# Kernel optimization log

Hardware: AMD Instinct MI355X
Metric: run time of the kernel (lower is better)

Reference implementation:

```python
import jax, jax.numpy as jnp
import numpy as np

B, S, F, U = 64, 512, 128, 512          # seq_length == units (required for broadcast in original code)
SIGDIM = F + F * F                       # level-2 truncated signature dimension
GRID_SIZE, SPLINE_ORDER = 5, 3           # efficient-KAN style defaults
NB = GRID_SIZE + SPLINE_ORDER            # number of b-spline basis functions per input feature
LN_EPS = 1e-3                            # keras LayerNormalization default epsilon


def _make_grid():
    h = 2.0 / GRID_SIZE  # uniform grid on [-1, 1], extended by spline order
    return -1.0 + h * jnp.arange(-SPLINE_ORDER, GRID_SIZE + SPLINE_ORDER + 1, dtype=jnp.float32)


def _b_splines(x, grid):
    # x: (N, F) -> (N, F, NB) via Cox-de Boor recursion
    x = x[..., None]
    bases = ((x >= grid[:-1]) & (x < grid[1:])).astype(x.dtype)
    for p in range(1, SPLINE_ORDER + 1):
        left = (x - grid[:-(p + 1)]) / (grid[p:-1] - grid[:-(p + 1)])
        right = (grid[p + 1:] - x) / (grid[p + 1:] - grid[1:-p])
        bases = left * bases[..., :-1] + right * bases[..., 1:]
    return bases


def _kan_linear(x, base_w, spline_w, grid):
    # KANLinear, no bias / no layernorm: silu base branch + b-spline branch
    lead = x.shape[:-1]
    base = jax.nn.silu(x) @ base_w                                  # (..., U)
    b = _b_splines(x.reshape(-1, x.shape[-1]), grid)                # (N, F, NB)
    spl = jnp.einsum('nfk,ufk->nu', b, spline_w).reshape(*lead, base_w.shape[1])
    return base + spl


def _signature2(x):
    # level-2 path signature of piecewise-linear path x: (B, S, F) -> (B, F + F*F)
    dx = x[:, 1:] - x[:, :-1]                                       # (B, S-1, F)
    s1 = dx.sum(axis=1)                                             # (B, F)
    cs = jnp.cumsum(dx, axis=1)
    prev = jnp.concatenate([jnp.zeros_like(cs[:, :1]), cs[:, :-1]], axis=1)
    s2 = jnp.einsum('bti,btj->bij', prev + 0.5 * dx, dx)            # (B, F, F)
    return jnp.concatenate([s1, s2.reshape(x.shape[0], -1)], axis=-1)


def _grkan(sig, w1, b1, w2, b2, w3, b3, w4, b4, ws, bs, gamma, beta):
    # gated residual network mapping signature -> softmax attention weights (B, U)
    h = jax.nn.elu(sig @ w1 + b1)
    h = h @ w2 + b2
    glu = jax.nn.sigmoid(h @ w3 + b3) * (h @ w4 + b4)
    y = sig @ ws + bs + glu
    mu = jnp.mean(y, axis=-1, keepdims=True)
    var = jnp.var(y, axis=-1, keepdims=True)
    y = (y - mu) / jnp.sqrt(var + LN_EPS) * gamma + beta
    return jax.nn.softmax(y, axis=-1)


def setup_inputs() -> dict:
    key = jax.random.key(0)
    ks = jax.random.split(key, 24)
    n = lambda k, shp, s=0.02: jax.random.normal(k, shp, dtype=jnp.float32) * s
    inp = {
        'inputs': jax.random.normal(ks[0], (B, S, F), dtype=jnp.float32),
        'h_prev': jax.random.normal(ks[1], (B, U), dtype=jnp.float32),
        'c_prev': jax.random.normal(ks[2], (B, U), dtype=jnp.float32),
        'time_kernel': n(ks[3], (S, 1), 0.1),
        'kan_base_w': n(ks[4], (F, U)),
        'kan_spline_w': n(ks[5], (U, F, NB)),
        'g_w1': n(ks[6], (SIGDIM, U)), 'g_b1': jnp.zeros((U,), jnp.float32),
        'g_w2': n(ks[7], (U, U)), 'g_b2': jnp.zeros((U,), jnp.float32),
        'g_w3': n(ks[8], (U, U)), 'g_b3': jnp.zeros((U,), jnp.float32),
        'g_w4': n(ks[9], (U, U)), 'g_b4': jnp.zeros((U,), jnp.float32),
        'g_skip_w': n(ks[10], (SIGDIM, U)), 'g_skip_b': jnp.zeros((U,), jnp.float32),
        'ln_gamma': jnp.ones((U,), jnp.float32), 'ln_beta': jnp.zeros((U,), jnp.float32),
        'wf': n(ks[11], (2 * U, U)), 'bf': jnp.zeros((U,), jnp.float32),
        'wi': n(ks[12], (2 * U, U)), 'bi': jnp.zeros((U,), jnp.float32),
        'wc': n(ks[13], (2 * U, U)), 'bc': jnp.zeros((U,), jnp.float32),
        'wo': n(ks[14], (2 * U, U)), 'bo': jnp.zeros((U,), jnp.float32),
    }
    return inp


def reference(inputs, h_prev, c_prev, time_kernel, kan_base_w, kan_spline_w,
              g_w1, g_b1, g_w2, g_b2, g_w3, g_b3, g_w4, g_b4, g_skip_w, g_skip_b,
              ln_gamma, ln_beta, wf, bf, wi, bi, wc, bc, wo, bo):
    grid = _make_grid()
    weighted = time_kernel * inputs                                  # (B,S,F)
    sig = _signature2(weighted)                                      # (B,SIGDIM)
    attn = _grkan(sig, g_w1, g_b1, g_w2, g_b2, g_w3, g_b3, g_w4, g_b4,
                  g_skip_w, g_skip_b, ln_gamma, ln_beta)             # (B,S) since U==S
    kan_out = _kan_linear(weighted, kan_base_w, kan_spline_w, grid)  # (B,S,U)
    attended = kan_out * attn[..., None]                             # (B,S,U)
    current = attended.mean(axis=1)                                  # (B,U)
    combined = jnp.concatenate([current, h_prev], axis=-1)           # (B,2U)
    f = jax.nn.sigmoid(combined @ wf + bf)
    i = jax.nn.sigmoid(combined @ wi + bi)
    cand = jnp.tanh(combined @ wc + bc)
    o = jax.nn.sigmoid(combined @ wo + bo)
    c_new = f * c_prev + i * cand
    h_new = o * jnp.tanh(c_new)
    return h_new, c_new
```

## Files before the change

kernel.cpp:

```cpp
#include <hip/hip_runtime.h>
#include <math.h>

#define BB 64
#define SS 512
#define FF 128
#define UU 512
#define SIGDIM (FF + FF*FF)
#define K3 16512
#define KK 1152
#define SIG_KC 43
#define SIG_STEPS 6

typedef __attribute__((ext_vector_type(8))) __bf16 bf16x8;
typedef __attribute__((ext_vector_type(8))) unsigned short u16x8;
typedef __attribute__((ext_vector_type(4))) float f32x4;

__device__ __forceinline__ unsigned short f2bf(float x) {
    unsigned int u = __float_as_uint(x);
    unsigned int r = u + 0x7FFFu + ((u >> 16) & 1u);
    return (unsigned short)(r >> 16);
}

__device__ __forceinline__ float sigmoidf(float x) { return 1.0f / (1.0f + expf(-x)); }

__global__ __launch_bounds__(256) void k_prep(const float* __restrict__ splw,
                                              const float* __restrict__ basew,
                                              const float* __restrict__ h_prev,
                                              const float* __restrict__ w2, const float* __restrict__ w3,
                                              const float* __restrict__ w4, const float* __restrict__ wf,
                                              const float* __restrict__ wi, const float* __restrict__ wc,
                                              const float* __restrict__ wo,
                                              unsigned short* __restrict__ Wt,
                                              unsigned short* __restrict__ comb_b,
                                              unsigned short* __restrict__ W2t,
                                              unsigned short* __restrict__ W3t,
                                              unsigned short* __restrict__ W4t,
                                              unsigned short* __restrict__ Wgt) {
    int z = blockIdx.z;
    int tid = threadIdx.x;
    if (z == 0) {
        int base = (blockIdx.y * 16 + blockIdx.x) * 256 + tid;
        {
            int b = base >> 9, uu = base & 511;
            comb_b[(size_t)b * 1024 + 512 + uu] = f2bf(h_prev[base]);
        }
        for (int idx = base; idx < UU * KK; idx += 128 * 256) {
            int u = idx / KK, c = idx % KK;
            float v = (c < 1024) ? splw[(size_t)u * 1024 + c] : basew[(size_t)(c - 1024) * UU + u];
            Wt[idx] = f2bf(v);
        }
        return;
    }
    int zz = z - 1;
    int Kdim = (zz < 3) ? 512 : 1024;
    int kt = blockIdx.x, ut = blockIdx.y;
    if (kt * 64 >= Kdim) return;
    const float* src;
    unsigned short* dst;
    switch (zz) {
        case 0: src = w2; dst = W2t; break;
        case 1: src = w3; dst = W3t; break;
        case 2: src = w4; dst = W4t; break;
        case 3: src = wf; dst = Wgt; break;
        case 4: src = wi; dst = Wgt + (size_t)512 * 1024; break;
        case 5: src = wc; dst = Wgt + (size_t)1024 * 1024; break;
        default: src = wo; dst = Wgt + (size_t)1536 * 1024; break;
    }
    __shared__ float tile[64][67];
    int k0 = kt * 64, u0 = ut * 64;
#pragma unroll
    for (int p = 0; p < 4; ++p) {
        int e = p * 256 + tid;
        int kk = e >> 4, c4 = (e & 15) * 4;
        const float4 v = *(const float4*)(src + (size_t)(k0 + kk) * UU + u0 + c4);
        tile[kk][c4 + 0] = v.x;
        tile[kk][c4 + 1] = v.y;
        tile[kk][c4 + 2] = v.z;
        tile[kk][c4 + 3] = v.w;
    }
    __syncthreads();
    int kk0 = (tid & 7) * 8;
#pragma unroll
    for (int p = 0; p < 2; ++p) {
        int uu = (tid >> 3) + p * 32;
        u16x8 ov;
#pragma unroll
        for (int j = 0; j < 8; ++j) ov[j] = f2bf(tile[kk0 + j][uu]);
        *(u16x8*)(dst + (size_t)(u0 + uu) * Kdim + k0 + kk0) = ov;
    }
}

__global__ __launch_bounds__(256) void k_adprep(const float* __restrict__ inp,
                                                const float* __restrict__ tk,
                                                unsigned short* __restrict__ aT,
                                                unsigned short* __restrict__ dT,
                                                unsigned short* __restrict__ wT) {
    int tt0 = blockIdx.x * 64, f0 = blockIdx.y * 64, b = blockIdx.z;
    __shared__ float wS[65][67];
    __shared__ float w0S[64];
    int tid = threadIdx.x;
    const float* ib = inp + (size_t)b * SS * FF;
    if (tid < 64) w0S[tid] = tk[0] * ib[f0 + tid];
#pragma unroll
    for (int p = 0; p < 5; ++p) {
        int e = p * 256 + tid;
        if (e < 65 * 16) {
            int row = e >> 4, c4 = (e & 15) * 4;
            int t = tt0 + row;
            if (t < SS) {
                float tkt = tk[t];
                const float4 v = *(const float4*)(ib + (size_t)t * FF + f0 + c4);
                wS[row][c4 + 0] = tkt * v.x;
                wS[row][c4 + 1] = tkt * v.y;
                wS[row][c4 + 2] = tkt * v.z;
                wS[row][c4 + 3] = tkt * v.w;
            } else {
                wS[row][c4 + 0] = 0.f;
                wS[row][c4 + 1] = 0.f;
                wS[row][c4 + 2] = 0.f;
                wS[row][c4 + 3] = 0.f;
            }
        }
    }
    __syncthreads();
    int t8 = (tid & 7) * 8;
#pragma unroll
    for (int p = 0; p < 2; ++p) {
        int ff = (tid >> 3) + p * 32;
        float w0 = w0S[ff];
        u16x8 av, dv, wv;
#pragma unroll
        for (int j = 0; j < 8; ++j) {
            int tt = t8 + j;
            float w = wS[tt][ff];
            float wn = wS[tt + 1][ff];
            bool valid = (tt0 + tt) < (SS - 1);
            float a = valid ? 0.5f * (w + wn) - w0 : 0.f;
            float d = valid ? wn - w : 0.f;
            av[j] = f2bf(a);
            dv[j] = f2bf(d);
            wv[j] = f2bf(w);
        }
        size_t o = ((size_t)b * FF + f0 + ff) * SS + tt0 + t8;
        *(u16x8*)(aT + o) = av;
        *(u16x8*)(dT + o) = dv;
        *(u16x8*)(wT + o) = wv;
    }
}

__global__ __launch_bounds__(256) void k_sig_mfma(const unsigned short* __restrict__ aT,
                                                  const unsigned short* __restrict__ dT,
                                                  float* __restrict__ s2part) {
    int kc = blockIdx.x, b = blockIdx.y;
    int tid = threadIdx.x, lane = tid & 63;
    int wv = __builtin_amdgcn_readfirstlane(tid >> 6);
    int wrow = (wv & 1) * 64, wcol = (wv >> 1) * 64;
    int k0 = kc * 128;
    const unsigned short* pa = aT + ((size_t)b * FF + wrow + (lane & 15)) * SS + k0 + (lane >> 4) * 8;
    const unsigned short* pd = dT + ((size_t)b * FF + wcol + (lane & 15)) * SS + k0 + (lane >> 4) * 8;
    f32x4 acc[4][4];
#pragma unroll
    for (int i = 0; i < 4; ++i)
#pragma unroll
        for (int j = 0; j < 4; ++j) acc[i][j] = (f32x4)(0.f);
#pragma unroll
    for (int t = 0; t < 4; ++t) {
        bf16x8 af[4], df[4];
#pragma unroll
        for (int rt = 0; rt < 4; ++rt) af[rt] = *(const bf16x8*)(pa + (size_t)rt * 16 * SS + t * 32);
#pragma unroll
        for (int ct = 0; ct < 4; ++ct) df[ct] = *(const bf16x8*)(pd + (size_t)ct * 16 * SS + t * 32);
#pragma unroll
        for (int rt = 0; rt < 4; ++rt)
#pragma unroll
            for (int ct = 0; ct < 4; ++ct)
                acc[rt][ct] = __builtin_amdgcn_mfma_f32_16x16x32_bf16(af[rt], df[ct], acc[rt][ct], 0, 0, 0);
    }
    float* outp = s2part + ((size_t)kc * BB + b) * (FF * FF);
    int quad = lane >> 4, col = lane & 15;
#pragma unroll
    for (int rt = 0; rt < 4; ++rt)
#pragma unroll
        for (int ct = 0; ct < 4; ++ct)
#pragma unroll
            for (int reg = 0; reg < 4; ++reg)
                outp[(wrow + rt * 16 + quad * 4 + reg) * FF + wcol + ct * 16 + col] = acc[rt][ct][reg];
}

__global__ void k_sig_reduce(const float* __restrict__ inp, const float* __restrict__ tk,
                             const float* __restrict__ s2part, unsigned short* __restrict__ sigb) {
    int idx = blockIdx.x * 256 + threadIdx.x;
    if (idx >= BB * SIGDIM) return;
    int b = idx / SIGDIM, r = idx % SIGDIM;
    float v;
    if (r < FF) {
        v = tk[SS - 1] * inp[((size_t)b * SS + SS - 1) * FF + r] - tk[0] * inp[(size_t)b * SS * FF + r];
    } else {
        int ij = r - FF;
        v = 0.f;
#pragma unroll
        for (int c = 0; c < 4; ++c) v += s2part[((size_t)c * BB + b) * (FF * FF) + ij];
    }
    sigb[idx] = f2bf(v);
}

__global__ __launch_bounds__(256) void k_sig_fused(const unsigned short* __restrict__ sigb,
                                                   const float* __restrict__ w1,
                                                   const float* __restrict__ gsw,
                                                   float* __restrict__ spart) {
    int nt = blockIdx.x, kc = blockIdx.y, mat = blockIdx.z;
    const float* src = mat ? gsw : w1;
    __shared__ float tile[64][67];
    int tid = threadIdx.x, lane = tid & 63;
    int wv = __builtin_amdgcn_readfirstlane(tid >> 6);
    int u0 = nt * 64;
    int n0 = wv * 16;
    int kbase = kc * (SIG_STEPS * 64);

    f32x4 acc[4];
#pragma unroll
    for (int i = 0; i < 4; ++i) acc[i] = (f32x4)(0.f);

    int nn = lane & 15;
    int kq = (lane >> 4) * 8;
    const unsigned short* pab = sigb + (size_t)nn * K3 + kq;

    for (int step = 0; step < SIG_STEPS; ++step) {
        int k0 = kbase + step * 64;
#pragma unroll
        for (int p = 0; p < 4; ++p) {
            int e = p * 256 + tid;
            int kk = e >> 4, c4 = (e & 15) * 4;
            const float4 v = *(const float4*)(src + (size_t)(k0 + kk) * UU + u0 + c4);
            tile[kk][c4 + 0] = v.x;
            tile[kk][c4 + 1] = v.y;
            tile[kk][c4 + 2] = v.z;
            tile[kk][c4 + 3] = v.w;
        }
        __syncthreads();
#pragma unroll
        for (int s = 0; s < 2; ++s) {
            u16x8 ub;
            int kb = s * 32 + kq;
#pragma unroll
            for (int j = 0; j < 8; ++j) ub[j] = f2bf(tile[kb + j][n0 + nn]);
            bf16x8 bfrag = __builtin_bit_cast(bf16x8, ub);
#pragma unroll
            for (int rt = 0; rt < 4; ++rt) {
                bf16x8 afrag = *(const bf16x8*)(pab + (size_t)(rt * 16) * K3 + k0 + s * 32);
                acc[rt] = __builtin_amdgcn_mfma_f32_16x16x32_bf16(afrag, bfrag, acc[rt], 0, 0, 0);
            }
        }
        __syncthreads();
    }

    int col = lane & 15, quad = lane >> 4;
    float* P = spart + ((size_t)(mat * SIG_KC + kc) * 64) * UU;
#pragma unroll
    for (int rt = 0; rt < 4; ++rt)
#pragma unroll
        for (int reg = 0; reg < 4; ++reg)
            P[(size_t)(rt * 16 + quad * 4 + reg) * UU + u0 + n0 + col] = acc[rt][reg];
}

__global__ __launch_bounds__(256) void k_sig_red2(const float* __restrict__ spart,
                                                  const float* __restrict__ b1,
                                                  unsigned short* __restrict__ h1b,
                                                  float* __restrict__ skippre) {
    int idx = blockIdx.x * 256 + threadIdx.x;
    int mat = idx >> 15;
    int rem = idx & 32767;
    int m = rem >> 9, n = rem & 511;
    const float* p = spart + ((size_t)(mat * SIG_KC) * 64 + m) * UU + n;
    float v = 0.f;
#pragma unroll
    for (int kc = 0; kc < SIG_KC; ++kc) v += p[(size_t)kc * 64 * UU];
    if (mat == 0) {
        v += b1[n];
        h1b[(size_t)m * UU + n] = f2bf(v > 0.f ? v : expf(v) - 1.0f);
    } else {
        skippre[(size_t)m * UU + n] = v;
    }
}

__global__ __launch_bounds__(64) void k_h2_direct(const unsigned short* __restrict__ h1b,
                                                  const unsigned short* __restrict__ W2t,
                                                  const float* __restrict__ b2,
                                                  unsigned short* __restrict__ h2b) {
    int lane = threadIdx.x;
    int mt = blockIdx.x, nt = blockIdx.y;
    const unsigned short* pa = h1b + (size_t)(mt * 16 + (lane & 15)) * 512 + (lane >> 4) * 8;
    const unsigned short* pb = W2t + (size_t)(nt * 16 + (lane & 15)) * 512 + (lane >> 4) * 8;
    f32x4 acc0 = (f32x4)(0.f), acc1 = (f32x4)(0.f);
#pragma unroll
    for (int t = 0; t < 16; t += 2) {
        bf16x8 a0 = *(const bf16x8*)(pa + t * 32);
        bf16x8 b0 = *(const bf16x8*)(pb + t * 32);
        bf16x8 a1 = *(const bf16x8*)(pa + t * 32 + 32);
        bf16x8 b1v = *(const bf16x8*)(pb + t * 32 + 32);
        acc0 = __builtin_amdgcn_mfma_f32_16x16x32_bf16(a0, b0, acc0, 0, 0, 0);
        acc1 = __builtin_amdgcn_mfma_f32_16x16x32_bf16(a1, b1v, acc1, 0, 0, 0);
    }
    int col = lane & 15, quad = lane >> 4;
    int j = nt * 16 + col;
    float bb = b2[j];
#pragma unroll
    for (int reg = 0; reg < 4; ++reg) {
        int row = mt * 16 + quad * 4 + reg;
        h2b[(size_t)row * UU + j] = f2bf(acc0[reg] + acc1[reg] + bb);
    }
}

__global__ __launch_bounds__(64) void k_glu_direct(const unsigned short* __restrict__ h2b,
                                                   const unsigned short* __restrict__ W3t,
                                                   const unsigned short* __restrict__ W4t,
                                                   const float* __restrict__ b3,
                                                   const float* __restrict__ b4,
                                                   const float* __restrict__ skippre,
                                                   const float* __restrict__ skb,
                                                   float* __restrict__ yv) {
    int lane = threadIdx.x;
    int mt = blockIdx.x, nt = blockIdx.y;
    const unsigned short* pa = h2b + (size_t)(mt * 16 + (lane & 15)) * 512 + (lane >> 4) * 8;
    const unsigned short* pb3 = W3t + (size_t)(nt * 16 + (lane & 15)) * 512 + (lane >> 4) * 8;
    const unsigned short* pb4 = W4t + (size_t)(nt * 16 + (lane & 15)) * 512 + (lane >> 4) * 8;
    f32x4 acc3 = (f32x4)(0.f), acc4 = (f32x4)(0.f);
#pragma unroll
    for (int t = 0; t < 16; ++t) {
        bf16x8 a = *(const bf16x8*)(pa + t * 32);
        bf16x8 b3f = *(const bf16x8*)(pb3 + t * 32);
        bf16x8 b4f = *(const bf16x8*)(pb4 + t * 32);
        acc3 = __builtin_amdgcn_mfma_f32_16x16x32_bf16(a, b3f, acc3, 0, 0, 0);
        acc4 = __builtin_amdgcn_mfma_f32_16x16x32_bf16(a, b4f, acc4, 0, 0, 0);
    }
    int col = lane & 15, quad = lane >> 4;
    int j = nt * 16 + col;
    float bb3 = b3[j], bb4 = b4[j], sb = skb[j];
#pragma unroll
    for (int reg = 0; reg < 4; ++reg) {
        int row = mt * 16 + quad * 4 + reg;
        float g = sigmoidf(acc3[reg] + bb3);
        yv[(size_t)row * UU + j] = skippre[(size_t)row * UU + j] + sb + g * (acc4[reg] + bb4);
    }
}

__device__ __forceinline__ float block_sum(float v, float* red) {
    int tid = threadIdx.x;
#pragma unroll
    for (int off = 32; off > 0; off >>= 1) v += __shfl_down(v, off);
    __syncthreads();
    if ((tid & 63) == 0) red[tid >> 6] = v;
    __syncthreads();
    float r = red[0];
#pragma unroll
    for (int i = 1; i < 8; ++i) r += red[i];
    return r;
}
__device__ __forceinline__ float block_max(float v, float* red) {
    int tid = threadIdx.x;
#pragma unroll
    for (int off = 32; off > 0; off >>= 1) v = fmaxf(v, __shfl_down(v, off));
    __syncthreads();
    if ((tid & 63) == 0) red[tid >> 6] = v;
    __syncthreads();
    float r = red[0];
#pragma unroll
    for (int i = 1; i < 8; ++i) r = fmaxf(r, red[i]);
    return r;
}

__global__ void k_lnsm(const float* __restrict__ yv, const float* __restrict__ gamma,
                       const float* __restrict__ beta, float* __restrict__ attn) {
    int b = blockIdx.x, u = threadIdx.x;
    __shared__ float red[8];
    float v = yv[(size_t)b * UU + u];
    float mu = block_sum(v, red) * (1.0f / UU);
    float d = v - mu;
    float var = block_sum(d * d, red) * (1.0f / UU);
    float z = d * rsqrtf(var + 1e-3f) * gamma[u] + beta[u];
    float m = block_max(z, red);
    float e = expf(z - m);
    float Z = block_sum(e, red);
    attn[(size_t)b * UU + u] = e / Z;
}

__global__ __launch_bounds__(256) void k_kan_red(const unsigned short* __restrict__ wT,
                                                 const float* __restrict__ attn,
                                                 unsigned short* __restrict__ Aredb) {
    int b = blockIdx.x;
    int lane = threadIdx.x & 63;
    int f = blockIdx.y * 4 + (threadIdx.x >> 6);

    const u16x8 wv = *(const u16x8*)(wT + ((size_t)b * FF + f) * SS + lane * 8);
    const float* ap = attn + (size_t)b * UU + lane * 8;
    float4 a0 = *(const float4*)ap;
    float4 a1 = *(const float4*)(ap + 4);

    float acc[9] = {};
#pragma unroll
    for (int s = 0; s < 8; ++s) {
        float w = __uint_as_float((unsigned int)wv[s] << 16);
        float a = (s < 4) ? ((s == 0) ? a0.x : (s == 1) ? a0.y : (s == 2) ? a0.z : a0.w)
                          : ((s == 4) ? a1.x : (s == 5) ? a1.y : (s == 6) ? a1.z : a1.w);
        float t = (w + 2.2f) * 2.5f;
        float cf = floorf(fminf(fmaxf(t, -2.f), 13.f));
        int c = (int)cf;
        float u = t - cf;
        float u2 = u * u, u3 = u2 * u;
        float p0 = u3 * (1.f / 6.f);
        float p1 = (-3.f * u3 + 3.f * u2 + 3.f * u + 1.f) * (1.f / 6.f);
        float p2 = (3.f * u3 - 6.f * u2 + 4.f) * (1.f / 6.f);
        float onemu = 1.f - u;
        float p3 = onemu * onemu * onemu * (1.f / 6.f);
#pragma unroll
        for (int k2 = 0; k2 < 8; ++k2) {
            int d = c - k2;
            float v = (d == 0) ? p0 : (d == 1) ? p1 : (d == 2) ? p2 : (d == 3) ? p3 : 0.f;
            acc[k2] += a * v;
        }
        acc[8] += a * (w * sigmoidf(w));
    }

#pragma unroll
    for (int off = 1; off < 64; off <<= 1) {
#pragma unroll
        for (int k = 0; k < 9; ++k) acc[k] += __shfl_xor(acc[k], off);
    }

    if (lane == 0) {
        const float sc = 1.0f / SS;
        u16x8 ov;
#pragma unroll
        for (int k = 0; k < 8; ++k) ov[k] = f2bf(acc[k] * sc);
        *(u16x8*)(Aredb + (size_t)b * KK + f * 8) = ov;
        Aredb[(size_t)b * KK + 1024 + f] = f2bf(acc[8] * sc);
    }
}

__global__ __launch_bounds__(64) void k_cur_direct(const unsigned short* __restrict__ Aredb,
                                                   const unsigned short* __restrict__ Wt,
                                                   unsigned short* __restrict__ comb_b) {
    int lane = threadIdx.x;
    int mt = blockIdx.x, nt = blockIdx.y;
    const unsigned short* pa = Aredb + (size_t)(mt * 16 + (lane & 15)) * KK + (lane >> 4) * 8;
    const unsigned short* pb = Wt + (size_t)(nt * 16 + (lane & 15)) * KK + (lane >> 4) * 8;
    f32x4 acc0 = (f32x4)(0.f), acc1 = (f32x4)(0.f);
#pragma unroll 6
    for (int t = 0; t < KK / 32; t += 2) {
        bf16x8 a0 = *(const bf16x8*)(pa + t * 32);
        bf16x8 b0 = *(const bf16x8*)(pb + t * 32);
        bf16x8 a1 = *(const bf16x8*)(pa + t * 32 + 32);
        bf16x8 b1v = *(const bf16x8*)(pb + t * 32 + 32);
        acc0 = __builtin_amdgcn_mfma_f32_16x16x32_bf16(a0, b0, acc0, 0, 0, 0);
        acc1 = __builtin_amdgcn_mfma_f32_16x16x32_bf16(a1, b1v, acc1, 0, 0, 0);
    }
    int col = lane & 15, quad = lane >> 4;
    int j = nt * 16 + col;
#pragma unroll
    for (int reg = 0; reg < 4; ++reg) {
        int row = mt * 16 + quad * 4 + reg;
        comb_b[(size_t)row * 1024 + j] = f2bf(acc0[reg] + acc1[reg]);
    }
}

__global__ __launch_bounds__(64) void k_gates_cell(const unsigned short* __restrict__ comb_b,
                                                   const unsigned short* __restrict__ Wgt,
                                                   const float* __restrict__ bf_,
                                                   const float* __restrict__ bi_,
                                                   const float* __restrict__ bc_,
                                                   const float* __restrict__ bo_,
                                                   const float* __restrict__ c_prev,
                                                   float* __restrict__ out) {
    int lane = threadIdx.x;
    int mt = blockIdx.x, jt = blockIdx.y;
    const unsigned short* pa = comb_b + (size_t)(mt * 16 + (lane & 15)) * 1024 + (lane >> 4) * 8;
    const unsigned short* pb0 = Wgt + (size_t)(0 * 512 + jt * 16 + (lane & 15)) * 1024 + (lane >> 4) * 8;
    const unsigned short* pb1 = Wgt + (size_t)(1 * 512 + jt * 16 + (lane & 15)) * 1024 + (lane >> 4) * 8;
    const unsigned short* pb2 = Wgt + (size_t)(2 * 512 + jt * 16 + (lane & 15)) * 1024 + (lane >> 4) * 8;
    const unsigned short* pb3 = Wgt + (size_t)(3 * 512 + jt * 16 + (lane & 15)) * 1024 + (lane >> 4) * 8;
    f32x4 accf = (f32x4)(0.f), acci = (f32x4)(0.f), accc = (f32x4)(0.f), acco = (f32x4)(0.f);
#pragma unroll 4
    for (int t = 0; t < 32; ++t) {
        bf16x8 a = *(const bf16x8*)(pa + t * 32);
        bf16x8 b0 = *(const bf16x8*)(pb0 + t * 32);
        bf16x8 b1 = *(const bf16x8*)(pb1 + t * 32);
        bf16x8 b2 = *(const bf16x8*)(pb2 + t * 32);
        bf16x8 b3 = *(const bf16x8*)(pb3 + t * 32);
        accf = __builtin_amdgcn_mfma_f32_16x16x32_bf16(a, b0, accf, 0, 0, 0);
        acci = __builtin_amdgcn_mfma_f32_16x16x32_bf16(a, b1, acci, 0, 0, 0);
        accc = __builtin_amdgcn_mfma_f32_16x16x32_bf16(a, b2, accc, 0, 0, 0);
        acco = __builtin_amdgcn_mfma_f32_16x16x32_bf16(a, b3, acco, 0, 0, 0);
    }
    int col = lane & 15, quad = lane >> 4;
    int j = jt * 16 + col;
    float bfv = bf_[j], biv = bi_[j], bcv = bc_[j], bov = bo_[j];
#pragma unroll
    for (int reg = 0; reg < 4; ++reg) {
        int row = mt * 16 + quad * 4 + reg;
        float f = sigmoidf(accf[reg] + bfv);
        float ii = sigmoidf(acci[reg] + biv);
        float cd = tanhf(accc[reg] + bcv);
        float o = sigmoidf(acco[reg] + bov);
        float cn = f * c_prev[(size_t)row * UU + j] + ii * cd;
        out[(size_t)row * UU + j] = o * tanhf(cn);
        out[(size_t)BB * UU + (size_t)row * UU + j] = cn;
    }
}

extern "C" void kernel_launch(void* const* d_in, const int* in_sizes, int n_in,
                              void* d_out, int out_size, void* d_ws, size_t ws_size,
                              hipStream_t stream) {
    const float* inp   = (const float*)d_in[0];
    const float* hprev = (const float*)d_in[1];
    const float* cprev = (const float*)d_in[2];
    const float* tk    = (const float*)d_in[3];
    const float* basew = (const float*)d_in[4];
    const float* splw  = (const float*)d_in[5];
    const float* gw1   = (const float*)d_in[6];
    const float* gb1   = (const float*)d_in[7];
    const float* gw2   = (const float*)d_in[8];
    const float* gb2   = (const float*)d_in[9];
    const float* gw3   = (const float*)d_in[10];
    const float* gb3   = (const float*)d_in[11];
    const float* gw4   = (const float*)d_in[12];
    const float* gb4   = (const float*)d_in[13];
    const float* gsw   = (const float*)d_in[14];
    const float* gsb   = (const float*)d_in[15];
    const float* lng   = (const float*)d_in[16];
    const float* lnb   = (const float*)d_in[17];
    const float* wf    = (const float*)d_in[18];
    const float* bf_   = (const float*)d_in[19];
    const float* wi    = (const float*)d_in[20];
    const float* bi_   = (const float*)d_in[21];
    const float* wc    = (const float*)d_in[22];
    const float* bc_   = (const float*)d_in[23];
    const float* wo    = (const float*)d_in[24];
    const float* bo_   = (const float*)d_in[25];
    float* out = (float*)d_out;

    float* ws = (float*)d_ws;
    size_t o = 0;
    unsigned short* Wt  = (unsigned short*)(ws + o); o += (size_t)UU * KK / 2;
    float* s2part   = ws + o; o += (size_t)4 * BB * FF * FF;
    unsigned short* aT = (unsigned short*)(ws + o); o += (size_t)BB * FF * SS / 2;
    unsigned short* dT = (unsigned short*)(ws + o); o += (size_t)BB * FF * SS / 2;
    unsigned short* wT = (unsigned short*)(ws + o); o += (size_t)BB * FF * SS / 2;
    unsigned short* sigb = (unsigned short*)(ws + o); o += (size_t)BB * K3 / 2;
    float* spart    = ws + o; o += (size_t)2 * SIG_KC * 64 * UU;
    float* skippre  = ws + o; o += (size_t)BB * UU;
    unsigned short* h1b = (unsigned short*)(ws + o); o += (size_t)BB * UU / 2;
    unsigned short* h2b = (unsigned short*)(ws + o); o += (size_t)BB * UU / 2;
    float* yv       = ws + o; o += (size_t)BB * UU;
    float* attn     = ws + o; o += (size_t)BB * UU;
    unsigned short* Aredb = (unsigned short*)(ws + o); o += (size_t)BB * KK / 2;
    unsigned short* W2t = (unsigned short*)(ws + o); o += (size_t)512 * 512 / 2;
    unsigned short* W3t = (unsigned short*)(ws + o); o += (size_t)512 * 512 / 2;
    unsigned short* W4t = (unsigned short*)(ws + o); o += (size_t)512 * 512 / 2;
    unsigned short* Wgt = (unsigned short*)(ws + o); o += (size_t)2048 * 1024 / 2;
    unsigned short* comb_b = (unsigned short*)(ws + o); o += (size_t)BB * 1024 / 2;
    (void)ws_size; (void)in_sizes; (void)n_in; (void)out_size;

    k_prep<<<dim3(16, 8, 8), 256, 0, stream>>>(splw, basew, hprev, gw2, gw3, gw4, wf, wi, wc, wo,
                                               Wt, comb_b, W2t, W3t, W4t, Wgt);
    k_adprep<<<dim3(8, 2, BB), 256, 0, stream>>>(inp, tk, aT, dT, wT);
    k_sig_mfma<<<dim3(4, BB), 256, 0, stream>>>(aT, dT, s2part);
    k_sig_reduce<<<(BB * SIGDIM + 255) / 256, 256, 0, stream>>>(inp, tk, s2part, sigb);
    k_sig_fused<<<dim3(8, SIG_KC, 2), 256, 0, stream>>>(sigb, gw1, gsw, spart);
    k_sig_red2<<<256, 256, 0, stream>>>(spart, gb1, h1b, skippre);
    k_h2_direct<<<dim3(4, 32), 64, 0, stream>>>(h1b, W2t, gb2, h2b);
    k_glu_direct<<<dim3(4, 32), 64, 0, stream>>>(h2b, W3t, W4t, gb3, gb4, skippre, gsb, yv);
    k_lnsm<<<BB, UU, 0, stream>>>(yv, lng, lnb, attn);
    k_kan_red<<<dim3(BB, FF / 4), 256, 0, stream>>>(wT, attn, Aredb);
    k_cur_direct<<<dim3(4, 32), 64, 0, stream>>>(Aredb, Wt, comb_b);
    k_gates_cell<<<dim3(4, 32), 64, 0, stream>>>(comb_b, Wgt, bf_, bi_, bc_, bo_, cprev, out);
}
```

Measured before the change: 255.8 us.

## Fuse signature GEMM with reduction and merge GRN h2/GLU kernels

```diff
diff --git a/kernel.cpp b/kernel.cpp
--- a/kernel.cpp
+++ b/kernel.cpp
@@ -148,60 +148,68 @@
     }
 }
 
-__global__ __launch_bounds__(256) void k_sig_mfma(const unsigned short* __restrict__ aT,
+__global__ __launch_bounds__(256) void k_sig_quad(const unsigned short* __restrict__ aT,
                                                   const unsigned short* __restrict__ dT,
-                                                  float* __restrict__ s2part) {
-    int kc = blockIdx.x, b = blockIdx.y;
+                                                  const float* __restrict__ inp,
+                                                  const float* __restrict__ tk,
+                                                  unsigned short* __restrict__ sigb) {
+    int q = blockIdx.x, b = blockIdx.y;
+    int qr = q & 1, qc = q >> 1;
+    __shared__ unsigned short aS[64][72];
+    __shared__ unsigned short dS[64][72];
     int tid = threadIdx.x, lane = tid & 63;
     int wv = __builtin_amdgcn_readfirstlane(tid >> 6);
-    int wrow = (wv & 1) * 64, wcol = (wv >> 1) * 64;
-    int k0 = kc * 128;
-    const unsigned short* pa = aT + ((size_t)b * FF + wrow + (lane & 15)) * SS + k0 + (lane >> 4) * 8;
-    const unsigned short* pd = dT + ((size_t)b * FF + wcol + (lane & 15)) * SS + k0 + (lane >> 4) * 8;
-    f32x4 acc[4][4];
-#pragma unroll
-    for (int i = 0; i < 4; ++i)
-#pragma unroll
-        for (int j = 0; j < 4; ++j) acc[i][j] = (f32x4)(0.f);
-#pragma unroll
-    for (int t = 0; t < 4; ++t) {
-        bf16x8 af[4], df[4];
-#pragma unroll
-        for (int rt = 0; rt < 4; ++rt) af[rt] = *(const bf16x8*)(pa + (size_t)rt * 16 * SS + t * 32);
-#pragma unroll
-        for (int ct = 0; ct < 4; ++ct) df[ct] = *(const bf16x8*)(pd + (size_t)ct * 16 * SS + t * 32);
-#pragma unroll
-        for (int rt = 0; rt < 4; ++rt)
-#pragma unroll
-            for (int ct = 0; ct < 4; ++ct)
-                acc[rt][ct] = __builtin_amdgcn_mfma_f32_16x16x32_bf16(af[rt], df[ct], acc[rt][ct], 0, 0, 0);
-    }
-    float* outp = s2part + ((size_t)kc * BB + b) * (FF * FF);
+    int rowoff = (wv & 1) * 32, coloff = (wv >> 1) * 32;
+    const unsigned short* pabase = aT + ((size_t)b * FF + qr * 64) * SS;
+    const unsigned short* pdbase = dT + ((size_t)b * FF + qc * 64) * SS;
+
+    f32x4 acc[2][2];
+#pragma unroll
+    for (int i = 0; i < 2; ++i)
+#pragma unroll
+        for (int j = 0; j < 2; ++j) acc[i][j] = (f32x4)(0.f);
+
+    int arow0 = rowoff + (lane & 15);
+    int drow0 = coloff + (lane & 15);
+    int kq = (lane >> 4) * 8;
+
+    for (int kc = 0; kc < 8; ++kc) {
+#pragma unroll
+        for (int p = 0; p < 2; ++p) {
+            int e = p * 256 + tid;
+            int row = e >> 3, k8 = (e & 7) * 8;
+            *(u16x8*)&aS[row][k8] = *(const u16x8*)(pabase + (size_t)row * SS + kc * 64 + k8);
+            *(u16x8*)&dS[row][k8] = *(const u16x8*)(pdbase + (size_t)row * SS + kc * 64 + k8);
+        }
+        __syncthreads();
+#pragma unroll
+        for (int ks = 0; ks < 2; ++ks) {
+            bf16x8 af0 = *(const bf16x8*)&aS[arow0][ks * 32 + kq];
+            bf16x8 af1 = *(const bf16x8*)&aS[arow0 + 16][ks * 32 + kq];
+            bf16x8 df0 = *(const bf16x8*)&dS[drow0][ks * 32 + kq];
+            bf16x8 df1 = *(const bf16x8*)&dS[drow0 + 16][ks * 32 + kq];
+            acc[0][0] = __builtin_amdgcn_mfma_f32_16x16x32_bf16(af0, df0, acc[0][0], 0, 0, 0);
+            acc[0][1] = __builtin_amdgcn_mfma_f32_16x16x32_bf16(af0, df1, acc[0][1], 0, 0, 0);
+            acc[1][0] = __builtin_amdgcn_mfma_f32_16x16x32_bf16(af1, df0, acc[1][0], 0, 0, 0);
+            acc[1][1] = __builtin_amdgcn_mfma_f32_16x16x32_bf16(af1, df1, acc[1][1], 0, 0, 0);
+        }
+        __syncthreads();
+    }
+
+    unsigned short* ob = sigb + (size_t)b * SIGDIM;
+    if (q == 0 && tid < FF) {
+        float v = tk[SS - 1] * inp[((size_t)b * SS + SS - 1) * FF + tid] - tk[0] * inp[(size_t)b * SS * FF + tid];
+        ob[tid] = f2bf(v);
+    }
     int quad = lane >> 4, col = lane & 15;
 #pragma unroll
-    for (int rt = 0; rt < 4; ++rt)
-#pragma unroll
-        for (int ct = 0; ct < 4; ++ct)
+    for (int rt = 0; rt < 2; ++rt)
+#pragma unroll
+        for (int ct = 0; ct < 2; ++ct)
 #pragma unroll
             for (int reg = 0; reg < 4; ++reg)
-                outp[(wrow + rt * 16 + quad * 4 + reg) * FF + wcol + ct * 16 + col] = acc[rt][ct][reg];
-}
-
-__global__ void k_sig_reduce(const float* __restrict__ inp, const float* __restrict__ tk,
-                             const float* __restrict__ s2part, unsigned short* __restrict__ sigb) {
-    int idx = blockIdx.x * 256 + threadIdx.x;
-    if (idx >= BB * SIGDIM) return;
-    int b = idx / SIGDIM, r = idx % SIGDIM;
-    float v;
-    if (r < FF) {
-        v = tk[SS - 1] * inp[((size_t)b * SS + SS - 1) * FF + r] - tk[0] * inp[(size_t)b * SS * FF + r];
-    } else {
-        int ij = r - FF;
-        v = 0.f;
-#pragma unroll
-        for (int c = 0; c < 4; ++c) v += s2part[((size_t)c * BB + b) * (FF * FF) + ij];
-    }
-    sigb[idx] = f2bf(v);
+                ob[FF + (qr * 64 + rowoff + rt * 16 + quad * 4 + reg) * FF
+                      + qc * 64 + coloff + ct * 16 + col] = f2bf(acc[rt][ct][reg]);
 }
 
 __global__ __launch_bounds__(256) void k_sig_fused(const unsigned short* __restrict__ sigb,
@@ -283,57 +291,52 @@
     }
 }
 
-__global__ __launch_bounds__(64) void k_h2_direct(const unsigned short* __restrict__ h1b,
-                                                  const unsigned short* __restrict__ W2t,
-                                                  const float* __restrict__ b2,
-                                                  unsigned short* __restrict__ h2b) {
+__global__ __launch_bounds__(64) void k_grn2(const unsigned short* __restrict__ h1b,
+                                             const unsigned short* __restrict__ W2t,
+                                             const float* __restrict__ b2,
+                                             const unsigned short* __restrict__ W3t,
+                                             const unsigned short* __restrict__ W4t,
+                                             const float* __restrict__ b3,
+                                             const float* __restrict__ b4,
+                                             const float* __restrict__ skippre,
+                                             const float* __restrict__ skb,
+                                             float* __restrict__ yv) {
     int lane = threadIdx.x;
     int mt = blockIdx.x, nt = blockIdx.y;
-    const unsigned short* pa = h1b + (size_t)(mt * 16 + (lane & 15)) * 512 + (lane >> 4) * 8;
-    const unsigned short* pb = W2t + (size_t)(nt * 16 + (lane & 15)) * 512 + (lane >> 4) * 8;
-    f32x4 acc0 = (f32x4)(0.f), acc1 = (f32x4)(0.f);
-#pragma unroll
-    for (int t = 0; t < 16; t += 2) {
-        bf16x8 a0 = *(const bf16x8*)(pa + t * 32);
-        bf16x8 b0 = *(const bf16x8*)(pb + t * 32);
-        bf16x8 a1 = *(const bf16x8*)(pa + t * 32 + 32);
-        bf16x8 b1v = *(const bf16x8*)(pb + t * 32 + 32);
-        acc0 = __builtin_amdgcn_mfma_f32_16x16x32_bf16(a0, b0, acc0, 0, 0, 0);
-        acc1 = __builtin_amdgcn_mfma_f32_16x16x32_bf16(a1, b1v, acc1, 0, 0, 0);
-    }
-    int col = lane & 15, quad = lane >> 4;
-    int j = nt * 16 + col;
-    float bb = b2[j];
-#pragma unroll
-    for (int reg = 0; reg < 4; ++reg) {
-        int row = mt * 16 + quad * 4 + reg;
-        h2b[(size_t)row * UU + j] = f2bf(acc0[reg] + acc1[reg] + bb);
-    }
-}
-
-__global__ __launch_bounds__(64) void k_glu_direct(const unsigned short* __restrict__ h2b,
-                                                   const unsigned short* __restrict__ W3t,
-                                                   const unsigned short* __restrict__ W4t,
-                                                   const float* __restrict__ b3,
-                                                   const float* __restrict__ b4,
-                                                   const float* __restrict__ skippre,
-                                                   const float* __restrict__ skb,
-                                                   float* __restrict__ yv) {
-    int lane = threadIdx.x;
-    int mt = blockIdx.x, nt = blockIdx.y;
-    const unsigned short* pa = h2b + (size_t)(mt * 16 + (lane & 15)) * 512 + (lane >> 4) * 8;
-    const unsigned short* pb3 = W3t + (size_t)(nt * 16 + (lane & 15)) * 512 + (lane >> 4) * 8;
-    const unsigned short* pb4 = W4t + (size_t)(nt * 16 + (lane & 15)) * 512 + (lane >> 4) * 8;
+    __shared__ unsigned short h2S[16][520];
+    int col = lane & 15, quad = lane >> 4, kq = quad * 8;
+
+    bf16x8 af[16];
+    const unsigned short* pa = h1b + (size_t)(mt * 16 + col) * 512 + kq;
+#pragma unroll
+    for (int t = 0; t < 16; ++t) af[t] = *(const bf16x8*)(pa + t * 32);
+
+    for (int ct = 0; ct < 32; ++ct) {
+        f32x4 acc = (f32x4)(0.f);
+        const unsigned short* pb = W2t + (size_t)(ct * 16 + col) * 512 + kq;
+#pragma unroll
+        for (int t = 0; t < 16; ++t) {
+            bf16x8 bf = *(const bf16x8*)(pb + t * 32);
+            acc = __builtin_amdgcn_mfma_f32_16x16x32_bf16(af[t], bf, acc, 0, 0, 0);
+        }
+        float bb = b2[ct * 16 + col];
+#pragma unroll
+        for (int reg = 0; reg < 4; ++reg)
+            h2S[quad * 4 + reg][ct * 16 + col] = f2bf(acc[reg] + bb);
+    }
+    __syncthreads();
+
     f32x4 acc3 = (f32x4)(0.f), acc4 = (f32x4)(0.f);
+    const unsigned short* pb3 = W3t + (size_t)(nt * 16 + col) * 512 + kq;
+    const unsigned short* pb4 = W4t + (size_t)(nt * 16 + col) * 512 + kq;
 #pragma unroll
     for (int t = 0; t < 16; ++t) {
-        bf16x8 a = *(const bf16x8*)(pa + t * 32);
+        bf16x8 a = *(const bf16x8*)&h2S[col][t * 32 + kq];
         bf16x8 b3f = *(const bf16x8*)(pb3 + t * 32);
         bf16x8 b4f = *(const bf16x8*)(pb4 + t * 32);
         acc3 = __builtin_amdgcn_mfma_f32_16x16x32_bf16(a, b3f, acc3, 0, 0, 0);
         acc4 = __builtin_amdgcn_mfma_f32_16x16x32_bf16(a, b4f, acc4, 0, 0, 0);
     }
-    int col = lane & 15, quad = lane >> 4;
     int j = nt * 16 + col;
     float bb3 = b3[j], bb4 = b4[j], sb = skb[j];
 #pragma unroll
@@ -541,7 +544,6 @@
     float* ws = (float*)d_ws;
     size_t o = 0;
     unsigned short* Wt  = (unsigned short*)(ws + o); o += (size_t)UU * KK / 2;
-    float* s2part   = ws + o; o += (size_t)4 * BB * FF * FF;
     unsigned short* aT = (unsigned short*)(ws + o); o += (size_t)BB * FF * SS / 2;
     unsigned short* dT = (unsigned short*)(ws + o); o += (size_t)BB * FF * SS / 2;
     unsigned short* wT = (unsigned short*)(ws + o); o += (size_t)BB * FF * SS / 2;
@@ -549,7 +551,6 @@
     float* spart    = ws + o; o += (size_t)2 * SIG_KC * 64 * UU;
     float* skippre  = ws + o; o += (size_t)BB * UU;
     unsigned short* h1b = (unsigned short*)(ws + o); o += (size_t)BB * UU / 2;
-    unsigned short* h2b = (unsigned short*)(ws + o); o += (size_t)BB * UU / 2;
     float* yv       = ws + o; o += (size_t)BB * UU;
     float* attn     = ws + o; o += (size_t)BB * UU;
     unsigned short* Aredb = (unsigned short*)(ws + o); o += (size_t)BB * KK / 2;
@@ -563,12 +564,10 @@
     k_prep<<<dim3(16, 8, 8), 256, 0, stream>>>(splw, basew, hprev, gw2, gw3, gw4, wf, wi, wc, wo,
                                                Wt, comb_b, W2t, W3t, W4t, Wgt);
     k_adprep<<<dim3(8, 2, BB), 256, 0, stream>>>(inp, tk, aT, dT, wT);
-    k_sig_mfma<<<dim3(4, BB), 256, 0, stream>>>(aT, dT, s2part);
-    k_sig_reduce<<<(BB * SIGDIM + 255) / 256, 256, 0, stream>>>(inp, tk, s2part, sigb);
+    k_sig_quad<<<dim3(4, BB), 256, 0, stream>>>(aT, dT, inp, tk, sigb);
     k_sig_fused<<<dim3(8, SIG_KC, 2), 256, 0, stream>>>(sigb, gw1, gsw, spart);
     k_sig_red2<<<256, 256, 0, stream>>>(spart, gb1, h1b, skippre);
-    k_h2_direct<<<dim3(4, 32), 64, 0, stream>>>(h1b, W2t, gb2, h2b);
-    k_glu_direct<<<dim3(4, 32), 64, 0, stream>>>(h2b, W3t, W4t, gb3, gb4, skippre, gsb, yv);
+    k_grn2<<<dim3(4, 32), 64, 0, stream>>>(h1b, W2t, gb2, W3t, W4t, gb3, gb4, skippre, gsb, yv);
     k_lnsm<<<BB, UU, 0, stream>>>(yv, lng, lnb, attn);
     k_kan_red<<<dim3(BB, FF / 4), 256, 0, stream>>>(wT, attn, Aredb);
     k_cur_direct<<<dim3(4, 32), 64, 0, stream>>>(Aredb, Wt, comb_b);
```

New measurement: 297.8 us. +16.4%, slower.
